# Optimization experiments

Hardware: AMD Instinct MI355X
Metric: run time of the kernel (lower is better)

Reference implementation:

```python
import jax, jax.numpy as jnp
import numpy as np

DIM = 180      # channel dim C
HEADS = 6      # num_heads
WS = 8         # window_size
HIDDEN = int(DIM * 4.0)  # mlp hidden = 720
HEAD_DIM = DIM // HEADS  # 30


def layernorm(x, scale, bias, eps=1e-5):
    m = jnp.mean(x, axis=-1, keepdims=True)
    v = jnp.var(x, axis=-1, keepdims=True)
    return (x - m) * jax.lax.rsqrt(v + eps) * scale + bias


def setup_inputs() -> dict:
    key = jax.random.key(0)
    ks = jax.random.split(key, 16)
    B, H, W = 4, 256, 256
    s = 0.02  # weight init scale for numerical sanity
    return {
        "x": jax.random.normal(ks[0], (B, H * W, DIM), jnp.float32),
        "norm1_scale": jnp.ones((DIM,), jnp.float32),
        "norm1_bias": jnp.zeros((DIM,), jnp.float32),
        "qkv_w": jax.random.normal(ks[1], (DIM, 3 * DIM), jnp.float32) * s,  # [in,out] == torch W.T
        "qkv_b": jax.random.normal(ks[2], (3 * DIM,), jnp.float32) * s,
        "proj_w": jax.random.normal(ks[3], (DIM, DIM), jnp.float32) * s,
        "proj_b": jax.random.normal(ks[4], (DIM,), jnp.float32) * s,
        "norm2_scale": jnp.ones((DIM,), jnp.float32),
        "norm2_bias": jnp.zeros((DIM,), jnp.float32),
        "mlp_w1": jax.random.normal(ks[5], (DIM, HIDDEN), jnp.float32) * s,
        "mlp_b1": jax.random.normal(ks[6], (HIDDEN,), jnp.float32) * s,
        "mlp_w2": jax.random.normal(ks[7], (HIDDEN, DIM), jnp.float32) * s,
        "mlp_b2": jax.random.normal(ks[8], (DIM,), jnp.float32) * s,
        "H": H,
        "W": W,
    }


def reference(x, norm1_scale, norm1_bias, qkv_w, qkv_b, proj_w, proj_b,
              norm2_scale, norm2_bias, mlp_w1, mlp_b1, mlp_w2, mlp_b2, H, W):
    B, L, C = x.shape
    shortcut = x
    h = layernorm(x, norm1_scale, norm1_bias).reshape(B, H, W, C)
    # pad to multiples of window size (no-op when H,W % WS == 0)
    pad_b = (WS - H % WS) % WS
    pad_r = (WS - W % WS) % WS
    h = jnp.pad(h, ((0, 0), (0, pad_b), (0, pad_r), (0, 0)))
    Hp, Wp = H + pad_b, W + pad_r
    # window_partition: (B,Hp,Wp,C) -> (nW*B, WS*WS, C)
    win = h.reshape(B, Hp // WS, WS, Wp // WS, WS, C)
    win = win.transpose(0, 1, 3, 2, 4, 5).reshape(-1, WS * WS, C)
    Bw, N, _ = win.shape
    # fused qkv projection
    qkv = (win @ qkv_w + qkv_b).reshape(Bw, N, 3, HEADS, HEAD_DIM)
    qkv = qkv.transpose(2, 0, 3, 1, 4)  # (3, Bw, heads, N, head_dim)
    q, k, v = qkv[0], qkv[1], qkv[2]
    q = q * (HEAD_DIM ** -0.5)
    attn = jax.nn.softmax(jnp.einsum('bhnd,bhmd->bhnm', q, k), axis=-1)
    o = jnp.einsum('bhnm,bhmd->bhnd', attn, v)
    o = o.transpose(0, 2, 1, 3).reshape(Bw, N, C)
    o = o @ proj_w + proj_b
    # window_reverse: (nW*B, WS*WS, C) -> (B,Hp,Wp,C)
    h = o.reshape(B, Hp // WS, Wp // WS, WS, WS, C)
    h = h.transpose(0, 1, 3, 2, 4, 5).reshape(B, Hp, Wp, C)
    h = h[:, :H, :W, :].reshape(B, H * W, C)
    x = shortcut + h
    # MLP with exact (erf) GELU, matching torch nn.GELU default
    y = layernorm(x, norm2_scale, norm2_bias)
    y = jax.nn.gelu(y @ mlp_w1 + mlp_b1, approximate=False) @ mlp_w2 + mlp_b2
    return x + y
```

## Files before the change

### kernel.cpp

```cpp
#include <hip/hip_runtime.h>

typedef unsigned int u32;
typedef unsigned short u16;
typedef __attribute__((ext_vector_type(8))) __bf16 bf16x8;
typedef __attribute__((ext_vector_type(4))) float f32x4;

#define MFMA(a,b,c) __builtin_amdgcn_mfma_f32_16x16x32_bf16(a,b,c,0,0,0)

__device__ __forceinline__ float bf2f(u16 v){ return __uint_as_float(((u32)v) << 16); }
__device__ __forceinline__ u16 f2bf(float f){
  u32 u = __float_as_uint(f);
  u += 0x7fffu + ((u >> 16) & 1u);
  return (u16)(u >> 16);
}
__device__ __forceinline__ u32 pack2(float a, float b){
  return (u32)f2bf(a) | ((u32)f2bf(b) << 16);
}
__device__ __forceinline__ float gelu_fast(float v){
  float t = v*(-1.5957691216f - 0.0713548163f*v*v);
  return v * __builtin_amdgcn_rcpf(1.f + __expf(t));
}

#define OQKV 0
#define OWP  122880
#define OW1  159744
#define OW2  307200
#define NW_TOT 495616

__global__ void swin_unpack(const float* __restrict__ qkvw, const float* __restrict__ projw,
                            const float* __restrict__ w1, const float* __restrict__ w2,
                            u16* __restrict__ ws){
  int idx = blockIdx.x * 256 + threadIdx.x;
  if (idx >= NW_TOT) return;
  float val = 0.f;
  if (idx < OWP){
    int t = idx, nt = t / 3072, r = t % 3072, kt = r >> 9, e = r & 511;
    int lane = e >> 3, j = e & 7;
    int n = nt*16 + (lane & 15), k = kt*32 + (lane >> 4)*8 + j;
    if (n < 576){
      int p = n / 192, c = n - p*192;
      if (c < 180 && k < 180) val = qkvw[k*540 + p*180 + c];
    }
  } else if (idx < OW1){
    int t = idx - OWP, nt = t / 3072, r = t % 3072, kt = r >> 9, e = r & 511;
    int lane = e >> 3, j = e & 7;
    int n = nt*16 + (lane & 15), k = kt*32 + (lane >> 4)*8 + j;
    if (n < 180 && k < 180) val = projw[k*180 + n];
  } else if (idx < OW2){
    int t = idx - OW1, nt = t / 3072, r = t % 3072, kt = r >> 9, e = r & 511;
    int lane = e >> 3, j = e & 7;
    int n = nt*16 + (lane & 15), k = kt*32 + (lane >> 4)*8 + j;
    if (n < 720 && k < 180) val = w1[k*720 + n];
  } else {
    int t = idx - OW2, nt = t / 11776, r = t % 11776, kt = r >> 9, e = r & 511;
    int lane = e >> 3, j = e & 7;
    int n = nt*16 + (lane & 15), k = kt*32 + (lane >> 4)*8 + j;
    if (n < 180 && k < 720) val = w2[k*180 + n];
  }
  ws[idx] = f2bf(val);
}

#define A_Y   0
#define A_Q   25600
#define A_K   51200
#define A_VT  76800
#define A_P   104448
#define A_RB  132096

__global__ __launch_bounds__(768, 1) void swin_attn(
    const float* __restrict__ x, const float* __restrict__ n1s, const float* __restrict__ n1b,
    const u16* __restrict__ ws, const float* __restrict__ qkvb,
    const float* __restrict__ projb, float* __restrict__ out){
  __shared__ __align__(16) char sm[132352];
  const int tid = threadIdx.x;
  const int w12 = tid >> 6, l = tid & 63, l15 = l & 15, lq = l >> 4;
  int* rb = (int*)(sm + A_RB);
  const f32x4 fz = {0.f, 0.f, 0.f, 0.f};

  if (tid < 64){
    int wb = blockIdx.x;
    int b = wb >> 10, wy = (wb >> 5) & 31, wx = wb & 31;
    rb[tid] = b*65536 + (wy*8 + (tid>>3))*256 + (wx*8 + (tid&7));
  }
  for (int i = tid; i < 2304; i += 768){
    int row = i / 36, t = i - row*36;
    if (t < 24){
      int buf = (t >= 12) ? A_K : A_Q; int tt = t % 12;
      *(u16*)(sm + buf + row*400 + ((tt>>1)*32 + 30 + (tt&1))*2) = 0;
    } else
      *(u16*)(sm + A_Y + row*400 + (180 + t - 24)*2) = 0;
  }
  __syncthreads();

  if (w12 < 8){
    int r3 = l & 7, lq2 = l >> 3;
    int n = w12*8 + r3;
    const float4* px = (const float4*)(x + (size_t)rb[n]*180);
    float4 v[6];
    #pragma unroll
    for (int i = 0; i < 5; ++i) v[i] = px[lq2 + 8*i];
    v[5] = (lq2 < 5) ? px[lq2 + 40] : make_float4(0.f,0.f,0.f,0.f);
    float s = 0.f, ss = 0.f;
    #pragma unroll
    for (int i = 0; i < 6; ++i){
      s  += v[i].x + v[i].y + v[i].z + v[i].w;
      ss += v[i].x*v[i].x + v[i].y*v[i].y + v[i].z*v[i].z + v[i].w*v[i].w;
    }
    #pragma unroll
    for (int m = 8; m <= 32; m <<= 1){ s += __shfl_xor(s, m); ss += __shfl_xor(ss, m); }
    float mean = s * (1.f/180.f);
    float rstd = rsqrtf(ss * (1.f/180.f) - mean*mean + 1e-5f);
    u32* yr = (u32*)(sm + A_Y + n*400);
    const float4* s4 = (const float4*)n1s;
    const float4* b4 = (const float4*)n1b;
    #pragma unroll
    for (int i = 0; i < 6; ++i){
      if (i < 5 || lq2 < 5){
        int c4 = lq2 + 8*i;
        float4 sc = s4[c4], bi = b4[c4];
        float e0 = (v[i].x - mean)*rstd*sc.x + bi.x;
        float e1 = (v[i].y - mean)*rstd*sc.y + bi.y;
        float e2 = (v[i].z - mean)*rstd*sc.z + bi.z;
        float e3 = (v[i].w - mean)*rstd*sc.w + bi.w;
        yr[c4*2]     = pack2(e0, e1);
        yr[c4*2 + 1] = pack2(e2, e3);
      }
    }
  }
  __syncthreads();

  {
    const int ntb = w12*3;
    f32x4 acc[4][3];
    #pragma unroll
    for (int m = 0; m < 4; ++m)
      #pragma unroll
      for (int i = 0; i < 3; ++i) acc[m][i] = fz;
    bf16x8 bcur[3];
    #pragma unroll
    for (int i = 0; i < 3; ++i)
      bcur[i] = *(const bf16x8*)(ws + OQKV + ((ntb+i)*6 + 0)*512 + l*8);
    #pragma unroll
    for (int kt = 0; kt < 6; ++kt){
      bf16x8 bnxt[3];
      if (kt < 5){
        #pragma unroll
        for (int i = 0; i < 3; ++i)
          bnxt[i] = *(const bf16x8*)(ws + OQKV + ((ntb+i)*6 + kt + 1)*512 + l*8);
      }
      bf16x8 a[4];
      #pragma unroll
      for (int m = 0; m < 4; ++m)
        a[m] = *(const bf16x8*)(sm + A_Y + (m*16 + l15)*400 + kt*64 + lq*16);
      #pragma unroll
      for (int m = 0; m < 4; ++m)
        #pragma unroll
        for (int i = 0; i < 3; ++i)
          acc[m][i] = MFMA(a[m], bcur[i], acc[m][i]);
      if (kt < 5){
        #pragma unroll
        for (int i = 0; i < 3; ++i) bcur[i] = bnxt[i];
      }
    }
    #pragma unroll
    for (int i = 0; i < 3; ++i){
      int n = (ntb + i)*16 + l15;
      int p = n / 192, c = n - p*192;
      if (c < 180){
        float bias = qkvb[p*180 + c];
        int h = c / 30, d = c - h*30;
        int colp = h*32 + d;
        #pragma unroll
        for (int m = 0; m < 4; ++m)
          #pragma unroll
          for (int r = 0; r < 4; ++r){
            float val = acc[m][i][r] + bias;
            int tok = m*16 + lq*4 + r;
            if (p == 0)      *(u16*)(sm + A_Q + tok*400 + colp*2) = f2bf(val * 0.18257418583505536f);
            else if (p == 1) *(u16*)(sm + A_K + tok*400 + colp*2) = f2bf(val);
            else             *(u16*)(sm + A_VT + colp*144 + tok*2) = f2bf(val);
          }
      }
    }
  }
  __syncthreads();

  {
    const int tq = w12 & 3, hbase = (w12 >> 2)*2;
    for (int h = hbase; h < hbase + 2; ++h){
      bf16x8 aq = *(const bf16x8*)(sm + A_Q + (tq*16 + l15)*400 + h*64 + lq*16);
      f32x4 s[4];
      #pragma unroll
      for (int nt = 0; nt < 4; ++nt){
        bf16x8 bk = *(const bf16x8*)(sm + A_K + (nt*16 + l15)*400 + h*64 + lq*16);
        s[nt] = MFMA(aq, bk, fz);
      }
      #pragma unroll
      for (int r = 0; r < 4; ++r){
        float mx = fmaxf(fmaxf(s[0][r], s[1][r]), fmaxf(s[2][r], s[3][r]));
        mx = fmaxf(mx, __shfl_xor(mx, 1));
        mx = fmaxf(mx, __shfl_xor(mx, 2));
        mx = fmaxf(mx, __shfl_xor(mx, 4));
        mx = fmaxf(mx, __shfl_xor(mx, 8));
        float e0 = __expf(s[0][r]-mx), e1 = __expf(s[1][r]-mx);
        float e2 = __expf(s[2][r]-mx), e3 = __expf(s[3][r]-mx);
        float sum = e0 + e1 + e2 + e3;
        sum += __shfl_xor(sum,1); sum += __shfl_xor(sum,2);
        sum += __shfl_xor(sum,4); sum += __shfl_xor(sum,8);
        float iv = 1.f / sum;
        char* pr = sm + A_P + w12*2304 + (lq*4 + r)*144 + l15*2;
        *(u16*)(pr)      = f2bf(e0 * iv);
        *(u16*)(pr + 32) = f2bf(e1 * iv);
        *(u16*)(pr + 64) = f2bf(e2 * iv);
        *(u16*)(pr + 96) = f2bf(e3 * iv);
      }
      asm volatile("s_waitcnt lgkmcnt(0)" ::: "memory");
      f32x4 o0 = fz, o1 = fz;
      #pragma unroll
      for (int kt = 0; kt < 2; ++kt){
        bf16x8 aP  = *(const bf16x8*)(sm + A_P + w12*2304 + l15*144 + kt*64 + lq*16);
        bf16x8 bv0 = *(const bf16x8*)(sm + A_VT + (h*32 + l15)*144 + kt*64 + lq*16);
        bf16x8 bv1 = *(const bf16x8*)(sm + A_VT + (h*32 + 16 + l15)*144 + kt*64 + lq*16);
        o0 = MFMA(aP, bv0, o0);
        o1 = MFMA(aP, bv1, o1);
      }
      #pragma unroll
      for (int r = 0; r < 4; ++r){
        int tok = tq*16 + lq*4 + r;
        {
          int col = h*30 + l15;
          *(u16*)(sm + A_Y + tok*400 + col*2) = f2bf(o0[r]);
        }
        if (l15 < 14){
          int col = h*30 + 16 + l15;
          *(u16*)(sm + A_Y + tok*400 + col*2) = f2bf(o1[r]);
        }
      }
    }
  }
  __syncthreads();

  {
    const int mh2 = w12 / 6, ng6 = w12 % 6;
    f32x4 acc[2][2];
    #pragma unroll
    for (int m = 0; m < 2; ++m)
      #pragma unroll
      for (int i = 0; i < 2; ++i) acc[m][i] = fz;
    bf16x8 bcur[2];
    #pragma unroll
    for (int i = 0; i < 2; ++i)
      bcur[i] = *(const bf16x8*)(ws + OWP + ((ng6*2+i)*6 + 0)*512 + l*8);
    #pragma unroll
    for (int kt = 0; kt < 6; ++kt){
      bf16x8 bnxt[2];
      if (kt < 5){
        #pragma unroll
        for (int i = 0; i < 2; ++i)
          bnxt[i] = *(const bf16x8*)(ws + OWP + ((ng6*2+i)*6 + kt + 1)*512 + l*8);
      }
      bf16x8 ah[2];
      #pragma unroll
      for (int m = 0; m < 2; ++m)
        ah[m] = *(const bf16x8*)(sm + A_Y + (mh2*32 + m*16 + l15)*400 + kt*64 + lq*16);
      #pragma unroll
      for (int m = 0; m < 2; ++m)
        #pragma unroll
        for (int i = 0; i < 2; ++i)
          acc[m][i] = MFMA(ah[m], bcur[i], acc[m][i]);
      if (kt < 5){
        #pragma unroll
        for (int i = 0; i < 2; ++i) bcur[i] = bnxt[i];
      }
    }
    float* res = (float*)(sm + A_Q);
    #pragma unroll
    for (int i = 0; i < 2; ++i){
      int col = (ng6*2 + i)*16 + l15;
      if (col < 180){
        float bias = projb[col];
        #pragma unroll
        for (int m = 0; m < 2; ++m)
          #pragma unroll
          for (int r = 0; r < 4; ++r)
            res[(mh2*32 + m*16 + lq*4 + r)*180 + col] = acc[m][i][r] + bias;
      }
    }
  }
  __syncthreads();

  {
    const float4* res4 = (const float4*)(sm + A_Q);
    for (int idx = tid; idx < 2880; idx += 768){
      int n = idx / 45, c4 = idx - n*45;
      size_t g4 = (size_t)rb[n]*45 + c4;
      float4 rv = res4[idx];
      float4 xv = ((const float4*)x)[g4];
      float4 o; o.x = rv.x + xv.x; o.y = rv.y + xv.y; o.z = rv.z + xv.z; o.w = rv.w + xv.w;
      ((float4*)out)[g4] = o;
    }
  }
}

#define M_Y 0
#define M_G 25600

__global__ __launch_bounds__(1024, 1) void swin_mlp(
    const float* __restrict__ n2s, const float* __restrict__ n2b,
    const u16* __restrict__ ws, const float* __restrict__ b1, const float* __restrict__ b2,
    float* __restrict__ out){
  __shared__ __align__(16) char sm[124928];
  const int tid = threadIdx.x;
  const int w16 = tid >> 6, l = tid & 63, l15 = l & 15, lq = l >> 4;
  const size_t base = (size_t)blockIdx.x * (64*180);
  const f32x4 fz = {0.f, 0.f, 0.f, 0.f};

  if (tid < 768){
    int row = tid / 12, col = 180 + tid % 12;
    *(u16*)(sm + M_Y + row*400 + col*2) = 0;
  }
  {
    int r4 = l & 3, lq4 = l >> 2;
    int n = w16*4 + r4;
    const float4* px = (const float4*)(out + base + (size_t)n*180);
    float4 v[3];
    v[0] = px[lq4];
    v[1] = px[lq4 + 16];
    v[2] = (lq4 < 13) ? px[lq4 + 32] : make_float4(0.f,0.f,0.f,0.f);
    float s = 0.f, ss = 0.f;
    #pragma unroll
    for (int i = 0; i < 3; ++i){
      s  += v[i].x + v[i].y + v[i].z + v[i].w;
      ss += v[i].x*v[i].x + v[i].y*v[i].y + v[i].z*v[i].z + v[i].w*v[i].w;
    }
    #pragma unroll
    for (int m = 4; m <= 32; m <<= 1){ s += __shfl_xor(s, m); ss += __shfl_xor(ss, m); }
    float mean = s * (1.f/180.f);
    float rstd = rsqrtf(ss * (1.f/180.f) - mean*mean + 1e-5f);
    u32* yr = (u32*)(sm + M_Y + n*400);
    const float4* s4 = (const float4*)n2s;
    const float4* b4 = (const float4*)n2b;
    #pragma unroll
    for (int i = 0; i < 3; ++i){
      if (i < 2 || lq4 < 13){
        int c4 = lq4 + 16*i;
        float4 sc = s4[c4], bi = b4[c4];
        float e0 = (v[i].x - mean)*rstd*sc.x + bi.x;
        float e1 = (v[i].y - mean)*rstd*sc.y + bi.y;
        float e2 = (v[i].z - mean)*rstd*sc.z + bi.z;
        float e3 = (v[i].w - mean)*rstd*sc.w + bi.w;
        yr[c4*2]     = pack2(e0, e1);
        yr[c4*2 + 1] = pack2(e2, e3);
      }
    }
  }
  __syncthreads();

  {
    const int ntb = w16*3;
    f32x4 acc[4][3];
    #pragma unroll
    for (int m = 0; m < 4; ++m)
      #pragma unroll
      for (int i = 0; i < 3; ++i) acc[m][i] = fz;
    bf16x8 bcur[3];
    #pragma unroll
    for (int i = 0; i < 3; ++i)
      bcur[i] = *(const bf16x8*)(ws + OW1 + ((ntb+i)*6 + 0)*512 + l*8);
    #pragma unroll
    for (int kt = 0; kt < 6; ++kt){
      bf16x8 bnxt[3];
      if (kt < 5){
        #pragma unroll
        for (int i = 0; i < 3; ++i)
          bnxt[i] = *(const bf16x8*)(ws + OW1 + ((ntb+i)*6 + kt + 1)*512 + l*8);
      }
      bf16x8 a[4];
      #pragma unroll
      for (int m = 0; m < 4; ++m)
        a[m] = *(const bf16x8*)(sm + M_Y + (m*16 + l15)*400 + kt*64 + lq*16);
      #pragma unroll
      for (int m = 0; m < 4; ++m)
        #pragma unroll
        for (int i = 0; i < 3; ++i)
          acc[m][i] = MFMA(a[m], bcur[i], acc[m][i]);
      if (kt < 5){
        #pragma unroll
        for (int i = 0; i < 3; ++i) bcur[i] = bnxt[i];
      }
    }
    #pragma unroll
    for (int i = 0; i < 3; ++i){
      int gc = (ntb + i)*16 + l15;
      float bias = (gc < 720) ? b1[gc] : 0.f;
      #pragma unroll
      for (int m = 0; m < 4; ++m)
        #pragma unroll
        for (int r = 0; r < 4; ++r){
          float v = acc[m][i][r] + bias;
          float gel = (gc < 720) ? gelu_fast(v) : 0.f;
          *(u16*)(sm + M_G + (m*16 + lq*4 + r)*1552 + gc*2) = f2bf(gel);
        }
    }
  }
  __syncthreads();

  {
    f32x4 acc2[4];
    #pragma unroll
    for (int m = 0; m < 4; ++m) acc2[m] = fz;
    bf16x8 wb0, wb1;
    wb0 = *(const bf16x8*)(ws + OW2 + (w16*23 + 0)*512 + l*8);
    wb1 = *(const bf16x8*)(ws + OW2 + (w16*23 + 1)*512 + l*8);
    for (int kt = 0; kt < 23; ++kt){
      int ktn = (kt < 21) ? kt + 2 : 22;
      bf16x8 wbn = *(const bf16x8*)(ws + OW2 + (w16*23 + ktn)*512 + l*8);
      bf16x8 a[4];
      #pragma unroll
      for (int m = 0; m < 4; ++m)
        a[m] = *(const bf16x8*)(sm + M_G + (m*16 + l15)*1552 + kt*64 + lq*16);
      #pragma unroll
      for (int m = 0; m < 4; ++m)
        acc2[m] = MFMA(a[m], wb0, acc2[m]);
      wb0 = wb1; wb1 = wbn;
    }
    __syncthreads();

    float* res = (float*)(sm + M_G);
    int col = w16*16 + l15;
    if (col < 180){
      float bias = b2[col];
      #pragma unroll
      for (int m = 0; m < 4; ++m)
        #pragma unroll
        for (int r = 0; r < 4; ++r)
          res[(m*16 + lq*4 + r)*180 + col] = acc2[m][r] + bias;
    }
  }
  __syncthreads();

  {
    const float4* res4 = (const float4*)(sm + M_G);
    float4* og = (float4*)(out + base);
    for (int idx = tid; idx < 2880; idx += 1024){
      float4 rv = res4[idx];
      float4 xv = og[idx];
      float4 o; o.x = rv.x + xv.x; o.y = rv.y + xv.y; o.z = rv.z + xv.z; o.w = rv.w + xv.w;
      og[idx] = o;
    }
  }
}

extern "C" void kernel_launch(void* const* d_in, const int* in_sizes, int n_in,
                              void* d_out, int out_size, void* d_ws, size_t ws_size,
                              hipStream_t stream){
  const float* x     = (const float*)d_in[0];
  const float* n1s   = (const float*)d_in[1];
  const float* n1b   = (const float*)d_in[2];
  const float* qkvw  = (const float*)d_in[3];
  const float* qkvb  = (const float*)d_in[4];
  const float* projw = (const float*)d_in[5];
  const float* projb = (const float*)d_in[6];
  const float* n2s   = (const float*)d_in[7];
  const float* n2b   = (const float*)d_in[8];
  const float* w1    = (const float*)d_in[9];
  const float* b1    = (const float*)d_in[10];
  const float* w2    = (const float*)d_in[11];
  const float* b2    = (const float*)d_in[12];
  float* outp = (float*)d_out;
  u16* wsp = (u16*)d_ws;

  swin_unpack<<<(NW_TOT + 255) / 256, 256, 0, stream>>>(qkvw, projw, w1, w2, wsp);
  swin_attn<<<4096, 768, 0, stream>>>(x, n1s, n1b, wsp, qkvb, projb, outp);
  swin_mlp<<<4096, 1024, 0, stream>>>(n2s, n2b, wsp, b1, b2, outp);
}
```

Baseline: 575.2 us.

## Widen attention kernel to 16 waves and repartition work per wave

Raises the attention kernel block from 12 to 16 wavefronts and redistributes every stage across them. LayerNorm uses 4 threads per row instead of 8, the QKV GEMM pads N to 48 tiles, attention loops over 24 (query-tile, head) units, and the projection gives each wave one 16-column tile. Weight buffers and shared memory grow to hold the padded layout. The aim is more latency hiding per CU, at the cost of wasted padded MFMA work and an uneven 24-over-16 split in the attention stage.

```diff
diff --git a/kernel.cpp b/kernel.cpp
--- a/kernel.cpp
+++ b/kernel.cpp
@@ -22,10 +22,10 @@
 }
 
 #define OQKV 0
-#define OWP  122880
-#define OW1  159744
-#define OW2  307200
-#define NW_TOT 495616
+#define OWP  147456
+#define OW1  196608
+#define OW2  344064
+#define NW_TOT 532480
 
 __global__ void swin_unpack(const float* __restrict__ qkvw, const float* __restrict__ projw,
                             const float* __restrict__ w1, const float* __restrict__ w2,
@@ -65,15 +65,15 @@
 #define A_K   51200
 #define A_VT  76800
 #define A_P   104448
-#define A_RB  132096
-
-__global__ __launch_bounds__(768, 1) void swin_attn(
+#define A_RB  141312
+
+__global__ __launch_bounds__(1024, 1) void swin_attn(
     const float* __restrict__ x, const float* __restrict__ n1s, const float* __restrict__ n1b,
     const u16* __restrict__ ws, const float* __restrict__ qkvb,
     const float* __restrict__ projb, float* __restrict__ out){
-  __shared__ __align__(16) char sm[132352];
+  __shared__ __align__(16) char sm[141568];
   const int tid = threadIdx.x;
-  const int w12 = tid >> 6, l = tid & 63, l15 = l & 15, lq = l >> 4;
+  const int w16 = tid >> 6, l = tid & 63, l15 = l & 15, lq = l >> 4;
   int* rb = (int*)(sm + A_RB);
   const f32x4 fz = {0.f, 0.f, 0.f, 0.f};
 
@@ -82,7 +82,7 @@
     int b = wb >> 10, wy = (wb >> 5) & 31, wx = wb & 31;
     rb[tid] = b*65536 + (wy*8 + (tid>>3))*256 + (wx*8 + (tid&7));
   }
-  for (int i = tid; i < 2304; i += 768){
+  for (int i = tid; i < 2304; i += 1024){
     int row = i / 36, t = i - row*36;
     if (t < 24){
       int buf = (t >= 12) ? A_K : A_Q; int tt = t % 12;
@@ -92,31 +92,31 @@
   }
   __syncthreads();
 
-  if (w12 < 8){
-    int r3 = l & 7, lq2 = l >> 3;
-    int n = w12*8 + r3;
+  {
+    int r4 = l & 3, lq4 = l >> 2;
+    int n = w16*4 + r4;
     const float4* px = (const float4*)(x + (size_t)rb[n]*180);
-    float4 v[6];
-    #pragma unroll
-    for (int i = 0; i < 5; ++i) v[i] = px[lq2 + 8*i];
-    v[5] = (lq2 < 5) ? px[lq2 + 40] : make_float4(0.f,0.f,0.f,0.f);
+    float4 v[3];
+    v[0] = px[lq4];
+    v[1] = px[lq4 + 16];
+    v[2] = (lq4 < 13) ? px[lq4 + 32] : make_float4(0.f,0.f,0.f,0.f);
     float s = 0.f, ss = 0.f;
     #pragma unroll
-    for (int i = 0; i < 6; ++i){
+    for (int i = 0; i < 3; ++i){
       s  += v[i].x + v[i].y + v[i].z + v[i].w;
       ss += v[i].x*v[i].x + v[i].y*v[i].y + v[i].z*v[i].z + v[i].w*v[i].w;
     }
     #pragma unroll
-    for (int m = 8; m <= 32; m <<= 1){ s += __shfl_xor(s, m); ss += __shfl_xor(ss, m); }
+    for (int m = 4; m <= 32; m <<= 1){ s += __shfl_xor(s, m); ss += __shfl_xor(ss, m); }
     float mean = s * (1.f/180.f);
     float rstd = rsqrtf(ss * (1.f/180.f) - mean*mean + 1e-5f);
     u32* yr = (u32*)(sm + A_Y + n*400);
     const float4* s4 = (const float4*)n1s;
     const float4* b4 = (const float4*)n1b;
     #pragma unroll
-    for (int i = 0; i < 6; ++i){
-      if (i < 5 || lq2 < 5){
-        int c4 = lq2 + 8*i;
+    for (int i = 0; i < 3; ++i){
+      if (i < 2 || lq4 < 13){
+        int c4 = lq4 + 16*i;
         float4 sc = s4[c4], bi = b4[c4];
         float e0 = (v[i].x - mean)*rstd*sc.x + bi.x;
         float e1 = (v[i].y - mean)*rstd*sc.y + bi.y;
@@ -130,7 +130,7 @@
   __syncthreads();
 
   {
-    const int ntb = w12*3;
+    const int ntb = w16*3;
     f32x4 acc[4][3];
     #pragma unroll
     for (int m = 0; m < 4; ++m)
@@ -165,29 +165,31 @@
     #pragma unroll
     for (int i = 0; i < 3; ++i){
       int n = (ntb + i)*16 + l15;
-      int p = n / 192, c = n - p*192;
-      if (c < 180){
-        float bias = qkvb[p*180 + c];
-        int h = c / 30, d = c - h*30;
-        int colp = h*32 + d;
-        #pragma unroll
-        for (int m = 0; m < 4; ++m)
+      if (n < 576){
+        int p = n / 192, c = n - p*192;
+        if (c < 180){
+          float bias = qkvb[p*180 + c];
+          int h = c / 30, d = c - h*30;
+          int colp = h*32 + d;
           #pragma unroll
-          for (int r = 0; r < 4; ++r){
-            float val = acc[m][i][r] + bias;
-            int tok = m*16 + lq*4 + r;
-            if (p == 0)      *(u16*)(sm + A_Q + tok*400 + colp*2) = f2bf(val * 0.18257418583505536f);
-            else if (p == 1) *(u16*)(sm + A_K + tok*400 + colp*2) = f2bf(val);
-            else             *(u16*)(sm + A_VT + colp*144 + tok*2) = f2bf(val);
-          }
-      }
-    }
-  }
-  __syncthreads();
-
-  {
-    const int tq = w12 & 3, hbase = (w12 >> 2)*2;
-    for (int h = hbase; h < hbase + 2; ++h){
+          for (int m = 0; m < 4; ++m)
+            #pragma unroll
+            for (int r = 0; r < 4; ++r){
+              float val = acc[m][i][r] + bias;
+              int tok = m*16 + lq*4 + r;
+              if (p == 0)      *(u16*)(sm + A_Q + tok*400 + colp*2) = f2bf(val * 0.18257418583505536f);
+              else if (p == 1) *(u16*)(sm + A_K + tok*400 + colp*2) = f2bf(val);
+              else             *(u16*)(sm + A_VT + colp*144 + tok*2) = f2bf(val);
+            }
+        }
+      }
+    }
+  }
+  __syncthreads();
+
+  {
+    for (int u = w16; u < 24; u += 16){
+      const int tq = u & 3, h = u >> 2;
       bf16x8 aq = *(const bf16x8*)(sm + A_Q + (tq*16 + l15)*400 + h*64 + lq*16);
       f32x4 s[4];
       #pragma unroll
@@ -208,7 +210,7 @@
         sum += __shfl_xor(sum,1); sum += __shfl_xor(sum,2);
         sum += __shfl_xor(sum,4); sum += __shfl_xor(sum,8);
         float iv = 1.f / sum;
-        char* pr = sm + A_P + w12*2304 + (lq*4 + r)*144 + l15*2;
+        char* pr = sm + A_P + w16*2304 + (lq*4 + r)*144 + l15*2;
         *(u16*)(pr)      = f2bf(e0 * iv);
         *(u16*)(pr + 32) = f2bf(e1 * iv);
         *(u16*)(pr + 64) = f2bf(e2 * iv);
@@ -218,7 +220,7 @@
       f32x4 o0 = fz, o1 = fz;
       #pragma unroll
       for (int kt = 0; kt < 2; ++kt){
-        bf16x8 aP  = *(const bf16x8*)(sm + A_P + w12*2304 + l15*144 + kt*64 + lq*16);
+        bf16x8 aP  = *(const bf16x8*)(sm + A_P + w16*2304 + l15*144 + kt*64 + lq*16);
         bf16x8 bv0 = *(const bf16x8*)(sm + A_VT + (h*32 + l15)*144 + kt*64 + lq*16);
         bf16x8 bv1 = *(const bf16x8*)(sm + A_VT + (h*32 + 16 + l15)*144 + kt*64 + lq*16);
         o0 = MFMA(aP, bv0, o0);
@@ -241,57 +243,39 @@
   __syncthreads();
 
   {
-    const int mh2 = w12 / 6, ng6 = w12 % 6;
-    f32x4 acc[2][2];
-    #pragma unroll
-    for (int m = 0; m < 2; ++m)
-      #pragma unroll
-      for (int i = 0; i < 2; ++i) acc[m][i] = fz;
-    bf16x8 bcur[2];
-    #pragma unroll
-    for (int i = 0; i < 2; ++i)
-      bcur[i] = *(const bf16x8*)(ws + OWP + ((ng6*2+i)*6 + 0)*512 + l*8);
+    f32x4 acc2[4];
+    #pragma unroll
+    for (int m = 0; m < 4; ++m) acc2[m] = fz;
+    bf16x8 wb0 = *(const bf16x8*)(ws + OWP + (w16*6 + 0)*512 + l*8);
     #pragma unroll
     for (int kt = 0; kt < 6; ++kt){
-      bf16x8 bnxt[2];
-      if (kt < 5){
-        #pragma unroll
-        for (int i = 0; i < 2; ++i)
-          bnxt[i] = *(const bf16x8*)(ws + OWP + ((ng6*2+i)*6 + kt + 1)*512 + l*8);
-      }
-      bf16x8 ah[2];
-      #pragma unroll
-      for (int m = 0; m < 2; ++m)
-        ah[m] = *(const bf16x8*)(sm + A_Y + (mh2*32 + m*16 + l15)*400 + kt*64 + lq*16);
-      #pragma unroll
-      for (int m = 0; m < 2; ++m)
-        #pragma unroll
-        for (int i = 0; i < 2; ++i)
-          acc[m][i] = MFMA(ah[m], bcur[i], acc[m][i]);
-      if (kt < 5){
-        #pragma unroll
-        for (int i = 0; i < 2; ++i) bcur[i] = bnxt[i];
-      }
+      bf16x8 wbn;
+      if (kt < 5) wbn = *(const bf16x8*)(ws + OWP + (w16*6 + kt + 1)*512 + l*8);
+      bf16x8 a[4];
+      #pragma unroll
+      for (int m = 0; m < 4; ++m)
+        a[m] = *(const bf16x8*)(sm + A_Y + (m*16 + l15)*400 + kt*64 + lq*16);
+      #pragma unroll
+      for (int m = 0; m < 4; ++m)
+        acc2[m] = MFMA(a[m], wb0, acc2[m]);
+      if (kt < 5) wb0 = wbn;
     }
     float* res = (float*)(sm + A_Q);
-    #pragma unroll
-    for (int i = 0; i < 2; ++i){
-      int col = (ng6*2 + i)*16 + l15;
-      if (col < 180){
-        float bias = projb[col];
-        #pragma unroll
-        for (int m = 0; m < 2; ++m)
-          #pragma unroll
-          for (int r = 0; r < 4; ++r)
-            res[(mh2*32 + m*16 + lq*4 + r)*180 + col] = acc[m][i][r] + bias;
-      }
+    int col = w16*16 + l15;
+    if (col < 180){
+      float bias = projb[col];
+      #pragma unroll
+      for (int m = 0; m < 4; ++m)
+        #pragma unroll
+        for (int r = 0; r < 4; ++r)
+          res[(m*16 + lq*4 + r)*180 + col] = acc2[m][r] + bias;
     }
   }
   __syncthreads();
 
   {
     const float4* res4 = (const float4*)(sm + A_Q);
-    for (int idx = tid; idx < 2880; idx += 768){
+    for (int idx = tid; idx < 2880; idx += 1024){
       int n = idx / 45, c4 = idx - n*45;
       size_t g4 = (size_t)rb[n]*45 + c4;
       float4 rv = res4[idx];
@@ -471,6 +455,6 @@
   u16* wsp = (u16*)d_ws;
 
   swin_unpack<<<(NW_TOT + 255) / 256, 256, 0, stream>>>(qkvw, projw, w1, w2, wsp);
-  swin_attn<<<4096, 768, 0, stream>>>(x, n1s, n1b, wsp, qkvb, projb, outp);
+  swin_attn<<<4096, 1024, 0, stream>>>(x, n1s, n1b, wsp, qkvb, projb, outp);
   swin_mlp<<<4096, 1024, 0, stream>>>(n2s, n2b, wsp, b1, b2, outp);
 }
```

After: 570.6 us. No clear change (-0.8%).
